# Performance work log

Measured on AMD Instinct MI355X. Metric: run time of the kernel, lower is better.

## Reference

```python
import jax, jax.numpy as jnp
import numpy as np

# Model / simulation constants (globals in the original repo)
B = 64
N_INPUTS = 784
N_HIDDEN = 2048
N_OUTPUTS = 10
N_NEURONS = N_HIDDEN + N_OUTPUTS
E = 262144          # number of recurrent edges
T_MAX = 30          # simulation steps
VMAX = 1.0
THRESH = 0.25
TAU = 5.0
DT = 0.5            # dt*vmax = 0.5 matches the 0.5-spaced delay grid


def setup_inputs() -> dict:
    key = jax.random.key(0)
    k = jax.random.split(key, 7)
    x = jax.random.normal(k[0], (B, N_INPUTS), jnp.float32)
    # recurrent edge list: sources are hidden neurons only (output rows zeroed in A),
    # targets may be any hidden or output neuron
    src = jax.random.randint(k[1], (E,), 0, N_HIDDEN)
    tgt = jax.random.randint(k[2], (E,), 0, N_NEURONS)
    # axonal delays drawn from arange(3.0, 8.0, 0.5) as in initialise_edges
    delays = jnp.arange(3.0, 8.0, 0.5, dtype=jnp.float32)
    L_e = delays[jax.random.randint(k[3], (E,), 0, delays.shape[0])]
    # signed uniform weights: uniform(0,1) * (+1/-1)
    sign = jnp.where(jax.random.uniform(k[4], (E,)) > 0.5, 1.0, -1.0).astype(jnp.float32)
    W_e = jax.random.uniform(k[5], (E,), dtype=jnp.float32) * sign
    input_W = (jax.random.uniform(k[6], (N_INPUTS, N_HIDDEN), dtype=jnp.float32,
                                  minval=-1.0, maxval=1.0) * 0.1)
    return {"x": x, "input_W": input_W, "W_e": W_e, "L_e": L_e,
            "src": src, "tgt": tgt}


def _snn_forward(x, input_W, W_e, L_e, src, tgt):
    # (B, n_hidden) input current, injected every 3rd step (phase == 2)
    input_currents = x @ input_W

    def step(carry, _):
        S, V, Vm, acc, phase = carry
        # edges whose traveling spike has reached its delay
        arrived = jnp.isclose(S, L_e, atol=1e-5, rtol=1e-8)          # (B, E) bool
        spikes = V * arrived * W_e                                   # (B, E)
        I_syn = jnp.zeros((B, N_NEURONS), spikes.dtype).at[:, tgt].add(spikes)
        I_syn = I_syn.at[:, :N_HIDDEN].add(jnp.where(phase == 2, input_currents, 0.0))
        # leaky integration
        Vm = Vm + (-Vm + I_syn) * (DT / TAU)
        V_exc = jnp.maximum(0.0, Vm - THRESH)
        fired = (V_exc > 0).at[:, -N_OUTPUTS:].set(False)            # outputs never spike
        # eval mode: dropout_rate == 0 -> no_dropout branch of lax.cond
        idle = S == 0
        newS = fired[:, src] & idle                                  # launch spike on idle edges
        S = S * ~arrived
        V = V * ~arrived
        acc = acc + Vm[:, -N_OUTPUTS:]
        Vm = Vm - Vm * fired - 0.2 * fired                           # reset + afterhyperpolarization
        S = S + (S > 0) * DT * VMAX + newS * DT * VMAX               # advance traveling spikes
        V = V + newS * V_exc[:, src]
        return (S, V, Vm, acc, (phase + 1) % 3), None

    carry0 = (jnp.zeros((B, E), jnp.float32),
              jnp.zeros((B, E), jnp.float32),
              jnp.zeros((B, N_NEURONS), jnp.float32),
              jnp.zeros((B, N_OUTPUTS), jnp.float32),
              jnp.asarray(0, jnp.int32))
    step_ck = jax.checkpoint(step, prevent_cse=False)
    (_, _, _, acc, _), _ = jax.lax.scan(step_ck, carry0, None, length=T_MAX)
    return acc / T_MAX


def reference(x, input_W, W_e, L_e, src, tgt):
    return _snn_forward(x, input_W, W_e, L_e, src, tgt)
```

## Files before the change

### kernel.cpp

```cpp
#include <hip/hip_runtime.h>
#include <hip/hip_cooperative_groups.h>

namespace cg = cooperative_groups;

static constexpr int B_    = 64;
static constexpr int NIN   = 784;
static constexpr int NH    = 2048;
static constexpr int NOUT  = 10;
static constexpr int NN    = 2058;
static constexpr int NE    = 262144;
static constexpr int CAP   = 208;
static constexpr int SB    = 128;
static constexpr int NRAIL = NH * 10;

static constexpr int PARTS = 4;
static constexpr int OWN   = 512;
static constexpr int STPB  = 1024;
static constexpr int GRID  = B_ * PARTS;

static constexpr size_t IC_OFF    = 0;
static constexpr size_t ERECT_OFF = IC_OFF + (size_t)B_ * NH;
static constexpr size_t CUR_OFF   = ERECT_OFF + 2ull * CAP * NN;
static constexpr size_t BAR_OFF   = CUR_OFF + NN + 8;
static constexpr size_t TABG_OFF  = (BAR_OFF + 64 * 16 + 63) & ~(size_t)63;

__device__ __forceinline__ float ld_agent(const float* p) {
    return __hip_atomic_load(p, __ATOMIC_RELAXED, __HIP_MEMORY_SCOPE_AGENT);
}
__device__ __forceinline__ void st_agent(float* p, float v) {
    __hip_atomic_store(p, v, __ATOMIC_RELAXED, __HIP_MEMORY_SCOPE_AGENT);
}

__device__ __forceinline__ void demux8(const float tv[8], const float w8[8],
                                       float Ia[6]) {
    #pragma unroll
    for (int u = 0; u < 8; ++u) {
        const unsigned uw = __float_as_uint(tv[u]);
        const int tau = uw & 7;
        const float vw = __uint_as_float(uw & ~7u) * w8[u];
        #pragma unroll
        for (int jt = 0; jt < 6; ++jt)
            Ia[jt] += (tau == jt) ? vw : 0.f;
    }
}

__device__ __forceinline__ void lds8(const float* __restrict__ tab,
                                     const int4 q[4], float tv[8], float w8[8]) {
    #pragma unroll
    for (int u = 0; u < 4; ++u) {
        tv[2 * u]     = *(const float*)((const char*)tab + q[u].x);
        tv[2 * u + 1] = *(const float*)((const char*)tab + q[u].z);
        w8[2 * u]     = __int_as_float(q[u].y);
        w8[2 * u + 1] = __int_as_float(q[u].w);
    }
}

__device__ __forceinline__ void gather_col(const int4* __restrict__ pcol,
                                           const float* __restrict__ tab,
                                           int deg, float Ia[6]) {
    const int it = (deg + 7) >> 3;
    if (it <= 0) return;
    const int4* p = pcol;
    int4 qc[4], qn[4];
    float tvp[8], wp[8], tvc[8], wc[8];
    #pragma unroll
    for (int u = 0; u < 4; ++u) qc[u] = p[(size_t)u * NN];
    lds8(tab, qc, tvp, wp);
    if (it > 1) {
        p += (size_t)4 * NN;
        #pragma unroll
        for (int u = 0; u < 4; ++u) qc[u] = p[(size_t)u * NN];
    }
    for (int i = 1; i < it; ++i) {
        if (i + 1 < it) {
            const int4* pn = p + (size_t)4 * NN;
            #pragma unroll
            for (int u = 0; u < 4; ++u) qn[u] = pn[(size_t)u * NN];
        }
        lds8(tab, qc, tvc, wc);
        demux8(tvp, wp, Ia);
        #pragma unroll
        for (int u = 0; u < 8; ++u) { tvp[u] = tvc[u]; wp[u] = wc[u]; }
        #pragma unroll
        for (int u = 0; u < 4; ++u) qc[u] = qn[u];
        p += (size_t)4 * NN;
    }
    demux8(tvp, wp, Ia);
}

__global__ __launch_bounds__(STPB, 4) void fused_kernel(
    const float* __restrict__ x, const float* __restrict__ inW,
    const int* __restrict__ src, const int* __restrict__ tgt,
    const float* __restrict__ We, const float* __restrict__ Le,
    float* __restrict__ IC, int* __restrict__ cnt,
    int2* __restrict__ erec2, int* __restrict__ bar,
    float* __restrict__ tabG, float* __restrict__ out)
{
    cg::grid_group grid = cg::this_grid();
    const int bid = blockIdx.x;
    const int tid = threadIdx.x;
    __shared__ float tab[NRAIL];
    __shared__ float cmb[6 * OWN];

    {
        float4* z = (float4*)erec2;
        const int n4 = (int)((2ull * CAP * NN + NN + 8 + 64 * 16 + 3) / 4);
        const int stride = GRID * STPB;
        for (int i = bid * STPB + tid; i < n4; i += stride)
            z[i] = float4{0.f, 0.f, 0.f, 0.f};
    }
    grid.sync();

    if (bid < SB) {
        int* lh    = (int*)tab;
        int* lbase = lh + NN;
        for (int i = tid; i < NN; i += STPB) lh[i] = 0;
        __syncthreads();
        const int base = bid * (NE / SB);
        for (int k = 0; k < NE / SB; k += STPB)
            atomicAdd(&lh[tgt[base + k + tid]], 1);
        __syncthreads();
        for (int i = tid; i < NN; i += STPB) {
            const int c = lh[i];
            lbase[i] = c ? atomicAdd(&cnt[i], c) : 0;
            lh[i] = 0;
        }
        __syncthreads();
        for (int k = 0; k < NE / SB; k += STPB) {
            const int e  = base + k + tid;
            const int tg = tgt[e];
            const int p  = lbase[tg] + atomicAdd(&lh[tg], 1);
            const int d  = (int)(Le[e] * 2.0f + 0.5f);
            if (p < CAP)
                erec2[((size_t)(p >> 1) * NN + tg) * 2 + (p & 1)] =
                    make_int2((src[e] + (d - 6) * NH) * 4,
                              __float_as_int(We[e]));
        }
    } else {
        const int gb = bid - SB;
        const int nc = gb & 7;
        const int bc = gb >> 3;
        const int sl = tid >> 8;
        const int t  = tid & 255;
        const int n  = nc * 256 + t;
        const int b0 = bc * 4 + sl;
        float a0 = 0.f;
        #pragma unroll 16
        for (int kk = 0; kk < NIN; ++kk)
            a0 = fmaf(x[b0 * NIN + kk], inW[(size_t)kk * NH + n], a0);
        IC[(size_t)b0 * NH + n] = a0;
    }
    grid.sync();

    const int b    = bid >> 2;
    const int part = bid & 3;
    const int lane = tid & 63;
    const int wv   = tid >> 6;
    const bool owner = tid < OWN;
    const int nl   = tid & (OWN - 1);

    const int4* __restrict__ erec4 = (const int4*)erec2;
    const int n    = part * OWN + nl;
    const int deg  = min(cnt[n], CAP);
    const int it   = (deg + 7) >> 3;
    const int hlow = (it + 1) >> 1;
    const float ic = owner ? IC[(size_t)b * NH + n] : 0.f;

    const bool oW = (part == 0 && wv < 8) || (part == 1 && wv < 2);
    const int o = (part == 0) ? wv : 8 + wv;
    const int degO = oW ? min(cnt[NH + o], CAP) : 0;

    int pa[10]; float pv[10];
    #pragma unroll
    for (int j = 0; j < 10; ++j) { pa[j] = -1; pv[j] = 0.f; }
    float Vm = 0.f, Vo = 0.f, acc = 0.f;

    int* const barb = bar + b * 16;

    for (int k = 0; k < 5; ++k) {
        const int t0 = 6 * k;
        float Ia[6] = {}, Io[6] = {};

        if (k) {
            if (tid == 0)
                while (__hip_atomic_load(barb, __ATOMIC_RELAXED,
                                         __HIP_MEMORY_SCOPE_AGENT) < 4 * k)
                    __builtin_amdgcn_s_sleep(1);
            __syncthreads();

            const float* gr = tabG + ((size_t)((k - 1) & 1) * B_ + b) * 10 * NH;
            #pragma unroll
            for (int j = 0; j < 10; ++j) {
                tab[j * NH + tid]        = ld_agent(gr + (size_t)j * NH + tid);
                tab[j * NH + 1024 + tid] = ld_agent(gr + (size_t)j * NH + 1024 + tid);
            }
            __syncthreads();

            if (owner) {
                gather_col(erec4 + n, tab, min(deg, 8 * hlow), Ia);
            } else {
                const int dh = deg - 8 * hlow;
                if (dh > 0)
                    gather_col(erec4 + n + (size_t)4 * NN * hlow, tab, dh, Ia);
            }
            if (oW) {
                const int2* __restrict__ e2 = (const int2*)erec4;
                for (int i = lane; i < degO; i += 64) {
                    const int2 r = e2[((size_t)(i >> 1) * NN + NH + o) * 2 + (i & 1)];
                    const unsigned uw =
                        __float_as_uint(*(const float*)((const char*)tab + r.x));
                    const int tau = uw & 7;
                    const float vw = __uint_as_float(uw & ~7u) * __int_as_float(r.y);
                    #pragma unroll
                    for (int jt = 0; jt < 6; ++jt)
                        Io[jt] += (tau == jt) ? vw : 0.f;
                }
                #pragma unroll
                for (int jt = 0; jt < 6; ++jt) {
                    #pragma unroll
                    for (int off = 32; off > 0; off >>= 1)
                        Io[jt] += __shfl_xor(Io[jt], off, 64);
                }
            }
            if (!owner) {
                #pragma unroll
                for (int jt = 0; jt < 6; ++jt) cmb[jt * OWN + nl] = Ia[jt];
            }
            __syncthreads();
            if (owner) {
                #pragma unroll
                for (int jt = 0; jt < 6; ++jt) Ia[jt] += cmb[jt * OWN + nl];
            }
        }

        if (owner) {
            #pragma unroll
            for (int j = 0; j < 6; ++j) {
                const int t = t0 + j;
                const bool inj = (j == 2 || j == 5);
                const float I = Ia[j] + (inj ? ic : 0.f);
                Vm += (I - Vm) * 0.1f;
                const float vx = fmaxf(Vm - 0.25f, 0.f);
                const bool f = vx > 0.f;
                #pragma unroll
                for (int jd = 0; jd < 10; ++jd)
                    if (f & (t > pa[jd])) { pa[jd] = t + jd + 6; pv[jd] = vx; }
                if (f) Vm = -0.2f;
                if (oW) { Vo += (Io[j] - Vo) * 0.1f; acc += Vo; }
            }
        }

        if (k < 4) {
            const int t0n = t0 + 6;
            float* gw = tabG + ((size_t)(k & 1) * B_ + b) * 10 * NH;
            if (owner) {
                #pragma unroll
                for (int j = 0; j < 10; ++j) {
                    const unsigned u1 = (unsigned)(pa[j] - t0n);
                    const unsigned c1 = (u1 < 6u) ? u1 : 7u;
                    st_agent(gw + (size_t)j * NH + n,
                             __uint_as_float((__float_as_uint(pv[j]) & ~7u) | c1));
                }
            }
            asm volatile("s_waitcnt vmcnt(0)" ::: "memory");
            __syncthreads();
            if (tid == 0)
                __hip_atomic_fetch_add(barb, 1, __ATOMIC_RELAXED,
                                       __HIP_MEMORY_SCOPE_AGENT);
        }
    }

    if (oW && lane == 0) out[b * NOUT + o] = acc * (1.0f / 30.0f);
}

extern "C" void kernel_launch(void* const* d_in, const int* in_sizes, int n_in,
                              void* d_out, int out_size, void* d_ws, size_t ws_size,
                              hipStream_t stream) {
    const float* x   = (const float*)d_in[0];
    const float* inW = (const float*)d_in[1];
    const float* We  = (const float*)d_in[2];
    const float* Le  = (const float*)d_in[3];
    const int*   src = (const int*)d_in[4];
    const int*   tgt = (const int*)d_in[5];

    float* ws    = (float*)d_ws;
    float* IC    = ws + IC_OFF;
    int2*  erec2 = (int2*)(ws + ERECT_OFF);
    int*   cnt   = (int*)(ws + CUR_OFF);
    int*   bar   = (int*)(ws + BAR_OFF);
    float* tabG  = ws + TABG_OFF;
    float* out   = (float*)d_out;

    void* kargs[] = { (void*)&x, (void*)&inW, (void*)&src, (void*)&tgt,
                      (void*)&We, (void*)&Le, (void*)&IC, (void*)&cnt,
                      (void*)&erec2, (void*)&bar, (void*)&tabG, (void*)&out };
    hipLaunchCooperativeKernel((const void*)fused_kernel,
                               dim3(GRID), dim3(STPB), kargs, 0, stream);
}
```

Baseline: 279.1 us.

## Sort gather work items by size across waves and keep own rail slice in LDS

Adds a per-block counting sort of (column, half) gather tasks by iteration count, so that threads in the same wavefront get similar trip counts and divergence in gather_col shrinks. Partial sums are written to a doubled shared combine buffer and summed by owners. Each block also writes its own freshly computed rail values directly into LDS and reloads only the other three parts' slices from global memory, cutting the reload traffic by a quarter. The cost is a one-time sort with several extra barriers, a larger shared buffer that may reduce occupancy, and an extra cnt load per gather.

```diff
diff --git a/kernel.cpp b/kernel.cpp
--- a/kernel.cpp
+++ b/kernel.cpp
@@ -100,7 +100,7 @@
     const int bid = blockIdx.x;
     const int tid = threadIdx.x;
     __shared__ float tab[NRAIL];
-    __shared__ float cmb[6 * OWN];
+    __shared__ float cmb[12 * OWN];
 
     {
         float4* z = (float4*)erec2;
@@ -159,11 +159,36 @@
     const bool owner = tid < OWN;
     const int nl   = tid & (OWN - 1);
 
+    int colA, halfA;
+    {
+        int* hist  = (int*)cmb;
+        int* curs  = hist + 16;
+        int* nrank = curs + 16;
+        if (tid < 16) { hist[tid] = 0; curs[tid] = 0; }
+        __syncthreads();
+        const int colI  = tid & (OWN - 1);
+        const int halfI = tid >> 9;
+        const int degI  = min(cnt[part * OWN + colI], CAP);
+        const int itI   = (degI + 7) >> 3;
+        const int hlI   = (itI + 1) >> 1;
+        const int szI   = halfI ? (itI - hlI) : hlI;
+        atomicAdd(&hist[szI], 1);
+        __syncthreads();
+        if (tid == 0) {
+            int s = 0;
+            for (int i = 0; i < 16; ++i) { const int c = hist[i]; hist[i] = s; s += c; }
+        }
+        __syncthreads();
+        const int r = hist[szI] + atomicAdd(&curs[szI], 1);
+        nrank[r] = tid;
+        __syncthreads();
+        const int item = nrank[tid];
+        colA = item & (OWN - 1); halfA = item >> 9;
+        __syncthreads();
+    }
+
     const int4* __restrict__ erec4 = (const int4*)erec2;
     const int n    = part * OWN + nl;
-    const int deg  = min(cnt[n], CAP);
-    const int it   = (deg + 7) >> 3;
-    const int hlow = (it + 1) >> 1;
     const float ic = owner ? IC[(size_t)b * NH + n] : 0.f;
 
     const bool oW = (part == 0 && wv < 8) || (part == 1 && wv < 2);
@@ -190,18 +215,33 @@
 
             const float* gr = tabG + ((size_t)((k - 1) & 1) * B_ + b) * 10 * NH;
             #pragma unroll
-            for (int j = 0; j < 10; ++j) {
-                tab[j * NH + tid]        = ld_agent(gr + (size_t)j * NH + tid);
-                tab[j * NH + 1024 + tid] = ld_agent(gr + (size_t)j * NH + 1024 + tid);
+            for (int i = 0; i < 15; ++i) {
+                const int f  = tid + i * STPB;
+                const int j  = f / 1536;
+                const int w2 = f - j * 1536;
+                const int qi = w2 >> 9;
+                const int fq = qi + (qi >= part ? 1 : 0);
+                const int c  = (w2 & (OWN - 1)) + fq * OWN;
+                tab[j * NH + c] = ld_agent(gr + (size_t)j * NH + c);
             }
             __syncthreads();
 
-            if (owner) {
-                gather_col(erec4 + n, tab, min(deg, 8 * hlow), Ia);
-            } else {
-                const int dh = deg - 8 * hlow;
-                if (dh > 0)
-                    gather_col(erec4 + n + (size_t)4 * NN * hlow, tab, dh, Ia);
+            {
+                float Ip[6] = {};
+                const int ng  = part * OWN + colA;
+                const int dg  = min(cnt[ng], CAP);
+                const int itg = (dg + 7) >> 3;
+                const int hlg = (itg + 1) >> 1;
+                if (halfA == 0) {
+                    gather_col(erec4 + ng, tab, min(dg, 8 * hlg), Ip);
+                } else {
+                    const int dh = dg - 8 * hlg;
+                    if (dh > 0)
+                        gather_col(erec4 + ng + (size_t)4 * NN * hlg, tab, dh, Ip);
+                }
+                #pragma unroll
+                for (int jt = 0; jt < 6; ++jt)
+                    cmb[(halfA * 6 + jt) * OWN + colA] = Ip[jt];
             }
             if (oW) {
                 const int2* __restrict__ e2 = (const int2*)erec4;
@@ -222,14 +262,11 @@
                         Io[jt] += __shfl_xor(Io[jt], off, 64);
                 }
             }
-            if (!owner) {
-                #pragma unroll
-                for (int jt = 0; jt < 6; ++jt) cmb[jt * OWN + nl] = Ia[jt];
-            }
             __syncthreads();
             if (owner) {
                 #pragma unroll
-                for (int jt = 0; jt < 6; ++jt) Ia[jt] += cmb[jt * OWN + nl];
+                for (int jt = 0; jt < 6; ++jt)
+                    Ia[jt] = cmb[jt * OWN + nl] + cmb[(6 + jt) * OWN + nl];
             }
         }
 
@@ -258,8 +295,10 @@
                 for (int j = 0; j < 10; ++j) {
                     const unsigned u1 = (unsigned)(pa[j] - t0n);
                     const unsigned c1 = (u1 < 6u) ? u1 : 7u;
-                    st_agent(gw + (size_t)j * NH + n,
-                             __uint_as_float((__float_as_uint(pv[j]) & ~7u) | c1));
+                    const float packed =
+                        __uint_as_float((__float_as_uint(pv[j]) & ~7u) | c1);
+                    tab[j * NH + n] = packed;
+                    st_agent(gw + (size_t)j * NH + n, packed);
                 }
             }
             asm volatile("s_waitcnt vmcnt(0)" ::: "memory");
```

Measured after the change: 318.0 us. 1.14x slower.

## Deepen gather prefetch and skip reloading block's own table slice

Applied to the files above, without the earlier changes.

The edge-record gather now prefetches two iterations ahead instead of one, so more global loads are in flight during the LDS lookups. Each block also writes its own partition's packed spike-table entries straight into shared memory, and the table refill loads only the other three partitions' columns from global memory. This cuts global refill traffic by a quarter and hides more gather latency, at the cost of extra registers and some index arithmetic per refill element.

```diff
diff --git a/kernel.cpp b/kernel.cpp
--- a/kernel.cpp
+++ b/kernel.cpp
@@ -60,30 +60,35 @@
                                            int deg, float Ia[6]) {
     const int it = (deg + 7) >> 3;
     if (it <= 0) return;
-    const int4* p = pcol;
-    int4 qc[4], qn[4];
+    int4 q0[4], qi[4], qi1[4];
     float tvp[8], wp[8], tvc[8], wc[8];
     #pragma unroll
-    for (int u = 0; u < 4; ++u) qc[u] = p[(size_t)u * NN];
-    lds8(tab, qc, tvp, wp);
+    for (int u = 0; u < 4; ++u) q0[u] = pcol[(size_t)u * NN];
     if (it > 1) {
-        p += (size_t)4 * NN;
-        #pragma unroll
-        for (int u = 0; u < 4; ++u) qc[u] = p[(size_t)u * NN];
-    }
+        const int4* p1 = pcol + (size_t)4 * NN;
+        #pragma unroll
+        for (int u = 0; u < 4; ++u) qi[u] = p1[(size_t)u * NN];
+    }
+    if (it > 2) {
+        const int4* p2 = pcol + (size_t)8 * NN;
+        #pragma unroll
+        for (int u = 0; u < 4; ++u) qi1[u] = p2[(size_t)u * NN];
+    }
+    lds8(tab, q0, tvp, wp);
+    const int4* pn = pcol + (size_t)12 * NN;
     for (int i = 1; i < it; ++i) {
-        if (i + 1 < it) {
-            const int4* pn = p + (size_t)4 * NN;
+        int4 qt[4];
+        if (i + 2 < it) {
             #pragma unroll
-            for (int u = 0; u < 4; ++u) qn[u] = pn[(size_t)u * NN];
-        }
-        lds8(tab, qc, tvc, wc);
+            for (int u = 0; u < 4; ++u) qt[u] = pn[(size_t)u * NN];
+        }
+        lds8(tab, qi, tvc, wc);
         demux8(tvp, wp, Ia);
         #pragma unroll
         for (int u = 0; u < 8; ++u) { tvp[u] = tvc[u]; wp[u] = wc[u]; }
         #pragma unroll
-        for (int u = 0; u < 4; ++u) qc[u] = qn[u];
-        p += (size_t)4 * NN;
+        for (int u = 0; u < 4; ++u) { qi[u] = qi1[u]; qi1[u] = qt[u]; }
+        pn += (size_t)4 * NN;
     }
     demux8(tvp, wp, Ia);
 }
@@ -190,9 +195,14 @@
 
             const float* gr = tabG + ((size_t)((k - 1) & 1) * B_ + b) * 10 * NH;
             #pragma unroll
-            for (int j = 0; j < 10; ++j) {
-                tab[j * NH + tid]        = ld_agent(gr + (size_t)j * NH + tid);
-                tab[j * NH + 1024 + tid] = ld_agent(gr + (size_t)j * NH + 1024 + tid);
+            for (int i = 0; i < 15; ++i) {
+                const int f  = tid + i * STPB;
+                const int j  = f / 1536;
+                const int w2 = f - j * 1536;
+                const int qi = w2 >> 9;
+                const int fq = qi + (qi >= part ? 1 : 0);
+                const int c  = (w2 & (OWN - 1)) + fq * OWN;
+                tab[j * NH + c] = ld_agent(gr + (size_t)j * NH + c);
             }
             __syncthreads();
 
@@ -258,8 +268,10 @@
                 for (int j = 0; j < 10; ++j) {
                     const unsigned u1 = (unsigned)(pa[j] - t0n);
                     const unsigned c1 = (u1 < 6u) ? u1 : 7u;
-                    st_agent(gw + (size_t)j * NH + n,
-                             __uint_as_float((__float_as_uint(pv[j]) & ~7u) | c1));
+                    const float packed =
+                        __uint_as_float((__float_as_uint(pv[j]) & ~7u) | c1);
+                    tab[j * NH + n] = packed;
+                    st_agent(gw + (size_t)j * NH + n, packed);
                 }
             }
             asm volatile("s_waitcnt vmcnt(0)" ::: "memory");
```

Measured after the change: 302.0 us. 8.2% more time.
